# Kernel optimization log

Measured on AMD Instinct MI355X. Metric: run time of the kernel, lower is better.

## Reference

```python
import jax, jax.numpy as jnp
import numpy as np

# TT factorization for fc1: 768 = 4*4*6*8 -> 3072 = 4*6*8*16, ranks (1,12,24,12,1)
# TT factorization for fc2: 3072 = 4*6*8*16 -> 768 = 4*4*6*8, ranks (1,12,24,12,1)
IN_F1, OUT_F1 = (4, 4, 6, 8), (4, 6, 8, 16)
IN_F2, OUT_F2 = (4, 6, 8, 16), (4, 4, 6, 8)
RANKS = (12, 24, 12)


def _core(key, shape, fan_in):
    return jax.random.normal(key, shape, dtype=jnp.float32) * (fan_in ** -0.5)


def make_tt_params(key, in_f, out_f, ranks):
    r = (1,) + tuple(ranks) + (1,)
    ks = jax.random.split(key, 5)
    # boundary cores squeeze the unit rank dims
    g1 = _core(ks[0], (in_f[0], out_f[0], r[1]), in_f[0])              # (i1,o1,r1)
    g2 = _core(ks[1], (r[1], in_f[1], out_f[1], r[2]), r[1] * in_f[1])  # (r1,i2,o2,r2)
    g3 = _core(ks[2], (r[2], in_f[2], out_f[2], r[3]), r[2] * in_f[2])  # (r2,i3,o3,r3)
    g4 = _core(ks[3], (r[3], in_f[3], out_f[3]), r[3] * in_f[3])        # (r3,i4,o4)
    b = jnp.zeros((int(np.prod(out_f)),), dtype=jnp.float32)
    return g1, g2, g3, g4, b


def tt_linear(x2d, g1, g2, g3, g4, bias, in_f):
    # x2d: (N, prod(in_f)) -> (N, prod(out_f))
    z = x2d.reshape((-1,) + tuple(in_f))                  # (b,i1,i2,i3,i4)
    z = jnp.einsum('bijkl,ipr->bjklpr', z, g1)            # (b,i2,i3,i4,o1,r1)
    z = jnp.einsum('bjklpr,rjqs->bklpqs', z, g2)          # (b,i3,i4,o1,o2,r2)
    z = jnp.einsum('bklpqs,sktu->blpqtu', z, g3)          # (b,i4,o1,o2,o3,r3)
    z = jnp.einsum('blpqtu,ulv->bpqtv', z, g4)            # (b,o1,o2,o3,o4)
    return z.reshape(z.shape[0], -1) + bias


def setup_inputs() -> dict:
    key = jax.random.key(0)
    kx, k1, k2 = jax.random.split(key, 3)
    x = jax.random.normal(kx, (2, 2048, 768), dtype=jnp.float32)
    g1a, g1b, g1c, g1d, b1 = make_tt_params(k1, IN_F1, OUT_F1, RANKS)
    g2a, g2b, g2c, g2d, b2 = make_tt_params(k2, IN_F2, OUT_F2, RANKS)
    return {"x": x, "g1a": g1a, "g1b": g1b, "g1c": g1c, "g1d": g1d, "b1": b1,
            "g2a": g2a, "g2b": g2b, "g2c": g2c, "g2d": g2d, "b2": b2}


def reference(x, g1a, g1b, g1c, g1d, b1, g2a, g2b, g2c, g2d, b2):
    B, S, D = x.shape
    h = tt_linear(x.reshape(-1, D), g1a, g1b, g1c, g1d, b1, IN_F1)  # (N, 3072)
    h = jax.nn.gelu(h, approximate=False)  # nn.GELU() default = exact erf
    # dropout: identity in eval mode
    y = tt_linear(h, g2a, g2b, g2c, g2d, b2, IN_F2)                 # (N, 768)
    return y.reshape(B, S, -1)
```

## Files before the change

kernel.cpp:

```cpp
#include <hip/hip_runtime.h>
#include <cstdint>
#include <cstddef>

typedef unsigned short u16;
typedef __attribute__((ext_vector_type(8))) __bf16 bf16x8;
typedef __attribute__((ext_vector_type(4))) float f32x4;

__device__ __forceinline__ u16 f2bf(float f) {
  unsigned u = __float_as_uint(f);
  u += 0x7FFFu + ((u >> 16) & 1u);
  return (u16)(u >> 16);
}

__device__ __forceinline__ float bf2f(u16 h) {
  return __uint_as_float(((unsigned)h) << 16);
}

__device__ __forceinline__ void async16(u16* lds, const u16* g) {
  __builtin_amdgcn_global_load_lds(
      (const __attribute__((address_space(1))) unsigned int*)g,
      (__attribute__((address_space(3))) unsigned int*)lds, 16, 0, 0);
}

__global__ __launch_bounds__(256)
void prep(const float4* __restrict__ x4, ushort4* __restrict__ xb4,
          const float* __restrict__ gA1, const float* __restrict__ gB1,
          const float* __restrict__ gC1, const float* __restrict__ gD1,
          const float* __restrict__ gA2, const float* __restrict__ gB2,
          const float* __restrict__ gC2, const float* __restrict__ gD2,
          float* __restrict__ B12_1, float* __restrict__ B12_2,
          float* __restrict__ C1, float* __restrict__ C2) {
  const int b = blockIdx.x;
  const int tid = threadIdx.x;
  if (b < 3072) {
    int i = b * 256 + tid;
    float4 v = x4[i];
    ushort4 o;
    o.x = f2bf(v.x); o.y = f2bf(v.y); o.z = f2bf(v.z); o.w = f2bf(v.w);
    xb4[i] = o;
    return;
  }
  int idx = (b - 3072) * 256 + tid;
  if (idx < 9216) {
    int e = idx;
    int r2 = e % 24; int t = e / 24;
    int fo12 = t % 24, fi12 = t / 24;
    int i2 = fi12 % 4, i1 = fi12 / 4;
    int o2 = fo12 % 6, o1 = fo12 / 6;
    float s = 0.f;
#pragma unroll
    for (int r1 = 0; r1 < 12; ++r1)
      s += gA1[(i1 * 4 + o1) * 12 + r1] * gB1[((r1 * 4 + i2) * 6 + o2) * 24 + r2];
    B12_1[e] = s;
  } else if (idx < 18432) {
    int e = idx - 9216;
    int r2 = e % 24; int t = e / 24;
    int fo12 = t % 16, fi12 = t / 16;
    int i2 = fi12 % 6, i1 = fi12 / 6;
    int o2 = fo12 % 4, o1 = fo12 / 4;
    float s = 0.f;
#pragma unroll
    for (int r1 = 0; r1 < 12; ++r1)
      s += gA2[(i1 * 4 + o1) * 12 + r1] * gB2[((r1 * 6 + i2) * 4 + o2) * 24 + r2];
    B12_2[e] = s;
  } else if (idx < 165888) {
    int e = idx - 18432;
    int fi34 = e % 48; int t = e / 48;
    int fo34 = t % 128;
    int i3 = fi34 / 8, i4 = fi34 % 8;
    int o3 = fo34 / 16, o4 = fo34 % 16;
    int r2 = t / 128;
    float s = 0.f;
#pragma unroll
    for (int r3 = 0; r3 < 12; ++r3)
      s += gC1[((r2 * 6 + i3) * 8 + o3) * 12 + r3] * gD1[(r3 * 8 + i4) * 16 + o4];
    C1[e] = s;
  } else {
    int e = idx - 165888;
    int fi34 = e % 128; int t = e / 128;
    int fo34 = t % 48;
    int i3 = fi34 / 16, i4 = fi34 % 16;
    int o3 = fo34 / 8, o4 = fo34 % 8;
    int r2 = t / 48;
    float s = 0.f;
#pragma unroll
    for (int r3 = 0; r3 < 12; ++r3)
      s += gC2[((r2 * 8 + i3) * 6 + o3) * 12 + r3] * gD2[(r3 * 16 + i4) * 8 + o4];
    C2[e] = s;
  }
}

template <int FI12, int I34, int O12, int O34, int OG>
__device__ __forceinline__
void tt_expand_body(const float* __restrict__ B12, const float* __restrict__ C34t,
                    u16* __restrict__ Wt, int bx, int by, int tid, float* sB) {
  constexpr int R2 = 24;
  constexpr int Kin = FI12 * I34;
  constexpr int IC = Kin / 8;
  constexpr int I34C = I34 / 8;
  for (int e = tid; e < FI12 * OG * R2; e += 256) {
    int r2 = e % R2; int t = e / R2;
    int f = t % OG; int fi12 = t / OG;
    sB[(fi12 * OG + f) * 25 + r2] = B12[(fi12 * O12 + by * OG + f) * R2 + r2];
  }
  __syncthreads();
  const int t = bx * 256 + tid;
  const int fo34 = t / IC;
  const int ic = t % IC;
  const int fi12 = ic / I34C;
  const int fi34 = (ic % I34C) * 8;

  float acc[OG][8];
#pragma unroll
  for (int f = 0; f < OG; ++f)
#pragma unroll
    for (int k = 0; k < 8; ++k) acc[f][k] = 0.f;

  for (int r2 = 0; r2 < R2; ++r2) {
    const float4* cp = (const float4*)(C34t + ((size_t)(r2 * O34 + fo34) * I34 + fi34));
    float4 c0 = cp[0], c1 = cp[1];
    float c[8] = {c0.x, c0.y, c0.z, c0.w, c1.x, c1.y, c1.z, c1.w};
#pragma unroll
    for (int f = 0; f < OG; ++f) {
      float bb = sB[(fi12 * OG + f) * 25 + r2];
#pragma unroll
      for (int k = 0; k < 8; ++k) acc[f][k] += bb * c[k];
    }
  }
#pragma unroll
  for (int f = 0; f < OG; ++f) {
    int out = (by * OG + f) * O34 + fo34;
    u16 v[8];
#pragma unroll
    for (int k = 0; k < 8; ++k) v[k] = f2bf(acc[f][k]);
    *(uint4*)(Wt + (size_t)out * Kin + fi12 * I34 + fi34) = *(const uint4*)v;
  }
}

__global__ __launch_bounds__(256)
void tt_expand2(const float* __restrict__ B12_1, const float* __restrict__ C1, u16* __restrict__ W1t,
                const float* __restrict__ B12_2, const float* __restrict__ C2, u16* __restrict__ W2t) {
  __shared__ float sB[24 * 4 * 25];
  const int b = blockIdx.x;
  const int tid = threadIdx.x;
  if (b < 288) {
    tt_expand_body<16, 48, 24, 128, 4>(B12_1, C1, W1t, b % 48, b / 48, tid, sB);
  } else {
    int bb = b - 288;
    tt_expand_body<24, 128, 16, 48, 4>(B12_2, C2, W2t, bb % 72, bb / 72, tid, sB);
  }
}

__global__ void reduceN8(const uint4* __restrict__ P, const float* __restrict__ bias,
                         float4* __restrict__ out4, int n8, int zstride8, int nz) {
  int i = blockIdx.x * 256 + threadIdx.x;
  if (i >= n8) return;
  int b0 = (i % 96) * 8;
  float a[8];
#pragma unroll
  for (int k = 0; k < 8; ++k) a[k] = bias[b0 + k];
  for (int s = 0; s < nz; ++s) {
    uint4 u = P[i + s * zstride8];
    const u16* up = (const u16*)&u;
#pragma unroll
    for (int k = 0; k < 8; ++k) a[k] += bf2f(up[k]);
  }
  out4[i * 2]     = (float4){a[0], a[1], a[2], a[3]};
  out4[i * 2 + 1] = (float4){a[4], a[5], a[6], a[7]};
}

template <bool GELU, int MAP>
__global__ __launch_bounds__(256, 3)
void gemm_bt(const u16* __restrict__ A, const u16* __restrict__ Bt,
             const float* __restrict__ bias, u16* __restrict__ Out,
             int N, int K, int klen, size_t zstride) {
  const int flat = blockIdx.x;
  const int xcd = flat & 7;
  const int local = flat >> 3;
  int bm, bn, bz;
  if (MAP == 1) {
    bm = (xcd >> 1) * 8 + (local & 7);
    bn = (xcd & 1) * 12 + (local >> 3);
    bz = 0;
  } else {
    bm = (xcd & 1) * 16 + (local & 15);
    bn = local >> 4;
    bz = xcd >> 1;
  }

  __shared__ __align__(16) u16 As[2][128 * 32];
  __shared__ __align__(16) u16 Bs[2][128 * 32];
  const int tid = threadIdx.x;
  const int wave = tid >> 6, lane = tid & 63;
  const int wm = (wave & 1) * 64, wn = (wave >> 1) * 64;
  const int lr = lane & 15, lq = lane >> 4;

  const int srow = tid >> 2;
  const int scol = (tid & 3) * 8;
  const u16* Ag = A + (size_t)(bm * 128 + srow) * K + scol;
  const u16* Bg = Bt + (size_t)(bn * 128 + srow) * K + scol;
  u16* AsW = &As[0][0] + tid * 8;
  u16* BsW = &Bs[0][0] + tid * 8;

  f32x4 acc[4][4];
#pragma unroll
  for (int i = 0; i < 4; i++)
#pragma unroll
    for (int j = 0; j < 4; j++) acc[i][j] = (f32x4){0.f, 0.f, 0.f, 0.f};

  const int kbeg = bz * klen;
  const int nIter = klen >> 5;

  auto stage = [&](int buf, int k0) {
    async16(AsW + buf * 4096,        Ag + k0);
    async16(AsW + buf * 4096 + 2048, Ag + k0 + (size_t)64 * K);
    async16(BsW + buf * 4096,        Bg + k0);
    async16(BsW + buf * 4096 + 2048, Bg + k0 + (size_t)64 * K);
  };
  auto compute = [&](int buf) {
    bf16x8 af[4], bfr[4];
#pragma unroll
    for (int i = 0; i < 4; i++)
      af[i] = *(const bf16x8*)(&As[buf][0] + (wm + i * 16 + lr) * 32 + lq * 8);
#pragma unroll
    for (int j = 0; j < 4; j++)
      bfr[j] = *(const bf16x8*)(&Bs[buf][0] + (wn + j * 16 + lr) * 32 + lq * 8);
#pragma unroll
    for (int i = 0; i < 4; i++)
#pragma unroll
      for (int j = 0; j < 4; j++)
        acc[i][j] = __builtin_amdgcn_mfma_f32_16x16x32_bf16(af[i], bfr[j], acc[i][j], 0, 0, 0);
  };

  stage(0, kbeg);
  for (int it = 0; it < nIter; it += 2) {
    __syncthreads();
    if (it + 1 < nIter) stage(1, kbeg + (it + 1) * 32);
    compute(0);
    __syncthreads();
    if (it + 2 < nIter) stage(0, kbeg + (it + 2) * 32);
    compute(1);
  }

  u16* Op = Out + (size_t)bz * zstride;
  const int r0 = bm * 128 + wm + lq * 4;
  const int c0 = bn * 128 + wn + lr;
  float bv[4];
  if (GELU) {
#pragma unroll
    for (int j = 0; j < 4; j++) bv[j] = bias[c0 + j * 16];
  }
#pragma unroll
  for (int i = 0; i < 4; i++) {
#pragma unroll
    for (int r = 0; r < 4; r++) {
      const size_t rowoff = (size_t)(r0 + i * 16 + r) * N;
#pragma unroll
      for (int j = 0; j < 4; j++) {
        float v = acc[i][j][r];
        if (GELU) {
          v += bv[j];
          float inner = v * fmaf(v * v, 0.0356774081f, 0.7978845608f);
          float e = __builtin_amdgcn_exp2f(2.8853900818f * inner);
          float r1 = __builtin_amdgcn_rcpf(1.0f + e);
          v = v - v * r1;
        }
        Op[rowoff + c0 + j * 16] = f2bf(v);
      }
    }
  }
}

extern "C" void kernel_launch(void* const* d_in, const int* in_sizes, int n_in,
                              void* d_out, int out_size, void* d_ws, size_t ws_size,
                              hipStream_t stream) {
  const float* x   = (const float*)d_in[0];
  const float* g1a = (const float*)d_in[1];
  const float* g1b = (const float*)d_in[2];
  const float* g1c = (const float*)d_in[3];
  const float* g1d = (const float*)d_in[4];
  const float* b1  = (const float*)d_in[5];
  const float* g2a = (const float*)d_in[6];
  const float* g2b = (const float*)d_in[7];
  const float* g2c = (const float*)d_in[8];
  const float* g2d = (const float*)d_in[9];
  const float* b2  = (const float*)d_in[10];
  float* out = (float*)d_out;

  char* ws = (char*)d_ws;
  u16* xb   = (u16*)(ws + 0);
  u16* W1t  = (u16*)(ws + 6291456);
  u16* W2t  = (u16*)(ws + 11010048);
  u16* h    = (u16*)(ws + 15728640);
  u16* Part = (u16*)(ws + 40894464);
  float* B12_1 = (float*)(ws + 40894464);
  float* B12_2 = (float*)(ws + 40894464 + 36864);
  float* C1    = (float*)(ws + 40894464 + 73728);
  float* C2    = (float*)(ws + 40894464 + 663552);

  prep<<<4296, 256, 0, stream>>>((const float4*)x, (ushort4*)xb,
                                 g1a, g1b, g1c, g1d, g2a, g2b, g2c, g2d,
                                 B12_1, B12_2, C1, C2);

  tt_expand2<<<576, 256, 0, stream>>>(B12_1, C1, W1t, B12_2, C2, W2t);

  gemm_bt<true, 1><<<768, 256, 0, stream>>>(xb, W1t, b1, h, 3072, 768, 768, 0);
  gemm_bt<false, 2><<<768, 256, 0, stream>>>(h, W2t, nullptr, Part, 768, 3072, 768, 3145728);
  reduceN8<<<1536, 256, 0, stream>>>((const uint4*)Part, b2,
                                     (float4*)out, 393216, 393216, 4);
}
```

Before: 159.7 us.

## Retile GEMMs to 256x192 blocks with 8 waves and phased LDS pipeline

Rewrites the bf16 GEMM kernel to use 512-thread blocks computing 256x192 tiles with a 64-wide K step. A/B tiles are double- and triple-buffered with an XOR swizzle to cut LDS bank conflicts. Each K step is split into four barrier-separated phases that interleave async global->LDS loads with MFMA bursts under raised wave priority. The aim is more data reuse per block and better overlap of memory with compute. The cost is higher register and LDS use and many more barriers, and the kernel now hardcodes K=768 per split (NT=12).

```diff
diff --git a/kernel.cpp b/kernel.cpp
--- a/kernel.cpp
+++ b/kernel.cpp
@@ -170,102 +170,180 @@
 }
 
 template <bool GELU, int MAP>
-__global__ __launch_bounds__(256, 3)
+__global__ __launch_bounds__(512, 2)
 void gemm_bt(const u16* __restrict__ A, const u16* __restrict__ Bt,
              const float* __restrict__ bias, u16* __restrict__ Out,
-             int N, int K, int klen, size_t zstride) {
+             int N, int lda, int ldb, size_t zstride) {
+  constexpr int NT = 12;
   const int flat = blockIdx.x;
   const int xcd = flat & 7;
   const int local = flat >> 3;
   int bm, bn, bz;
   if (MAP == 1) {
-    bm = (xcd >> 1) * 8 + (local & 7);
-    bn = (xcd & 1) * 12 + (local >> 3);
+    bm = (xcd >> 1) * 4 + (local & 3);
+    bn = (xcd & 1) * 8 + (local >> 2);
     bz = 0;
   } else {
-    bm = (xcd & 1) * 16 + (local & 15);
-    bn = local >> 4;
     bz = xcd >> 1;
-  }
-
-  __shared__ __align__(16) u16 As[2][128 * 32];
-  __shared__ __align__(16) u16 Bs[2][128 * 32];
+    bm = (xcd & 1) * 8 + (local & 7);
+    bn = local >> 3;
+  }
+  const int kbeg = (MAP == 2) ? bz * 768 : 0;
+
+  __shared__ __align__(16) u16 AL[2][16384];
+  __shared__ __align__(16) u16 BL[3][12288];
+
   const int tid = threadIdx.x;
   const int wave = tid >> 6, lane = tid & 63;
-  const int wm = (wave & 1) * 64, wn = (wave >> 1) * 64;
   const int lr = lane & 15, lq = lane >> 4;
-
-  const int srow = tid >> 2;
-  const int scol = (tid & 3) * 8;
-  const u16* Ag = A + (size_t)(bm * 128 + srow) * K + scol;
-  const u16* Bg = Bt + (size_t)(bn * 128 + srow) * K + scol;
-  u16* AsW = &As[0][0] + tid * 8;
-  u16* BsW = &Bs[0][0] + tid * 8;
-
-  f32x4 acc[4][4];
-#pragma unroll
-  for (int i = 0; i < 4; i++)
-#pragma unroll
-    for (int j = 0; j < 4; j++) acc[i][j] = (f32x4){0.f, 0.f, 0.f, 0.f};
-
-  const int kbeg = bz * klen;
-  const int nIter = klen >> 5;
-
-  auto stage = [&](int buf, int k0) {
-    async16(AsW + buf * 4096,        Ag + k0);
-    async16(AsW + buf * 4096 + 2048, Ag + k0 + (size_t)64 * K);
-    async16(BsW + buf * 4096,        Bg + k0);
-    async16(BsW + buf * 4096 + 2048, Bg + k0 + (size_t)64 * K);
+  const int wr = (wave >> 2) * 128;
+  const int wc = (wave & 3) * 48;
+
+  const int prow = tid >> 3;
+  const int pcc  = (tid & 7) ^ (((tid >> 5) & 1) << 1);
+  const u16* Ag = A + (size_t)(bm * 256 + prow) * lda + kbeg + pcc * 8;
+  const u16* Bg = Bt + (size_t)(bn * 192 + prow) * ldb + kbeg + pcc * 8;
+
+  auto stA = [&](int slot, int p, int k) {
+    async16(&AL[slot][0] + p * 4096 + tid * 8, Ag + (size_t)(p * 64) * lda + k);
   };
-  auto compute = [&](int buf) {
-    bf16x8 af[4], bfr[4];
-#pragma unroll
-    for (int i = 0; i < 4; i++)
-      af[i] = *(const bf16x8*)(&As[buf][0] + (wm + i * 16 + lr) * 32 + lq * 8);
-#pragma unroll
-    for (int j = 0; j < 4; j++)
-      bfr[j] = *(const bf16x8*)(&Bs[buf][0] + (wn + j * 16 + lr) * 32 + lq * 8);
-#pragma unroll
-    for (int i = 0; i < 4; i++)
-#pragma unroll
-      for (int j = 0; j < 4; j++)
-        acc[i][j] = __builtin_amdgcn_mfma_f32_16x16x32_bf16(af[i], bfr[j], acc[i][j], 0, 0, 0);
+  auto stB = [&](int slot, int p, int k) {
+    async16(&BL[slot][0] + p * 4096 + tid * 8, Bg + (size_t)(p * 64) * ldb + k);
   };
 
-  stage(0, kbeg);
-  for (int it = 0; it < nIter; it += 2) {
-    __syncthreads();
-    if (it + 1 < nIter) stage(1, kbeg + (it + 1) * 32);
-    compute(0);
-    __syncthreads();
-    if (it + 2 < nIter) stage(0, kbeg + (it + 2) * 32);
-    compute(1);
+  int aOff[2][8], bOff[2][3];
+#pragma unroll
+  for (int kk = 0; kk < 2; ++kk) {
+#pragma unroll
+    for (int mi = 0; mi < 8; ++mi) {
+      int L = (wr + mi * 16 + lr) * 128 + kk * 64 + lq * 16;
+      L ^= ((L >> 9) & 1) << 5;
+      aOff[kk][mi] = L >> 1;
+    }
+#pragma unroll
+    for (int nj = 0; nj < 3; ++nj) {
+      int L = (wc + nj * 16 + lr) * 128 + kk * 64 + lq * 16;
+      L ^= ((L >> 9) & 1) << 5;
+      bOff[kk][nj] = L >> 1;
+    }
+  }
+
+  f32x4 acc[8][3];
+#pragma unroll
+  for (int mi = 0; mi < 8; ++mi)
+#pragma unroll
+    for (int nj = 0; nj < 3; ++nj) acc[mi][nj] = (f32x4){0.f, 0.f, 0.f, 0.f};
+
+  stA(0, 0, 0); stA(0, 1, 0); stA(0, 2, 0); stA(0, 3, 0);
+  stB(0, 0, 0); stB(0, 1, 0); stB(0, 2, 0);
+  stB(1, 0, 64); stB(1, 1, 64); stB(1, 2, 64);
+  asm volatile("s_waitcnt vmcnt(3)" ::: "memory");
+  __builtin_amdgcn_s_barrier();
+  __builtin_amdgcn_sched_barrier(0);
+
+  int bsR = 0, bsW = 2;
+  for (int t = 0; t < NT; ++t) {
+    const u16* Ab = &AL[t & 1][0];
+    const u16* Bb = &BL[bsR][0];
+    const int wAs = (t + 1) & 1;
+    const int kA = ((t + 1 < NT) ? t + 1 : NT - 1) * 64;
+    const int kB = ((t + 2 < NT) ? t + 2 : NT - 1) * 64;
+
+    bf16x8 bf[3], af[4], af2[4];
+#pragma unroll
+    for (int nj = 0; nj < 3; ++nj) bf[nj] = *(const bf16x8*)(Bb + bOff[0][nj]);
+#pragma unroll
+    for (int mi = 0; mi < 4; ++mi) af[mi] = *(const bf16x8*)(Ab + aOff[0][mi]);
+    stA(wAs, 0, kA); stA(wAs, 1, kA);
+    __builtin_amdgcn_s_barrier();
+    asm volatile("s_waitcnt lgkmcnt(0)" ::: "memory");
+    __builtin_amdgcn_sched_barrier(0);
+    __builtin_amdgcn_s_setprio(1);
+#pragma unroll
+    for (int mi = 0; mi < 4; ++mi)
+#pragma unroll
+      for (int nj = 0; nj < 3; ++nj)
+        acc[mi][nj] = __builtin_amdgcn_mfma_f32_16x16x32_bf16(af[mi], bf[nj], acc[mi][nj], 0, 0, 0);
+    __builtin_amdgcn_s_setprio(0);
+    __builtin_amdgcn_s_barrier();
+    __builtin_amdgcn_sched_barrier(0);
+#pragma unroll
+    for (int mi = 0; mi < 4; ++mi) af2[mi] = *(const bf16x8*)(Ab + aOff[0][4 + mi]);
+    stA(wAs, 2, kA); stA(wAs, 3, kA);
+    __builtin_amdgcn_s_barrier();
+    asm volatile("s_waitcnt lgkmcnt(0)" ::: "memory");
+    __builtin_amdgcn_sched_barrier(0);
+    __builtin_amdgcn_s_setprio(1);
+#pragma unroll
+    for (int mi = 0; mi < 4; ++mi)
+#pragma unroll
+      for (int nj = 0; nj < 3; ++nj)
+        acc[4 + mi][nj] = __builtin_amdgcn_mfma_f32_16x16x32_bf16(af2[mi], bf[nj], acc[4 + mi][nj], 0, 0, 0);
+    __builtin_amdgcn_s_setprio(0);
+    __builtin_amdgcn_s_barrier();
+    __builtin_amdgcn_sched_barrier(0);
+#pragma unroll
+    for (int nj = 0; nj < 3; ++nj) bf[nj] = *(const bf16x8*)(Bb + bOff[1][nj]);
+#pragma unroll
+    for (int mi = 0; mi < 4; ++mi) af[mi] = *(const bf16x8*)(Ab + aOff[1][mi]);
+    stB(bsW, 0, kB); stB(bsW, 1, kB);
+    __builtin_amdgcn_s_barrier();
+    asm volatile("s_waitcnt lgkmcnt(0)" ::: "memory");
+    __builtin_amdgcn_sched_barrier(0);
+    __builtin_amdgcn_s_setprio(1);
+#pragma unroll
+    for (int mi = 0; mi < 4; ++mi)
+#pragma unroll
+      for (int nj = 0; nj < 3; ++nj)
+        acc[mi][nj] = __builtin_amdgcn_mfma_f32_16x16x32_bf16(af[mi], bf[nj], acc[mi][nj], 0, 0, 0);
+    __builtin_amdgcn_s_setprio(0);
+    __builtin_amdgcn_s_barrier();
+    __builtin_amdgcn_sched_barrier(0);
+#pragma unroll
+    for (int mi = 0; mi < 4; ++mi) af2[mi] = *(const bf16x8*)(Ab + aOff[1][4 + mi]);
+    stB(bsW, 2, kB);
+    __builtin_amdgcn_s_barrier();
+    asm volatile("s_waitcnt lgkmcnt(0)" ::: "memory");
+    __builtin_amdgcn_sched_barrier(0);
+    __builtin_amdgcn_s_setprio(1);
+#pragma unroll
+    for (int mi = 0; mi < 4; ++mi)
+#pragma unroll
+      for (int nj = 0; nj < 3; ++nj)
+        acc[4 + mi][nj] = __builtin_amdgcn_mfma_f32_16x16x32_bf16(af2[mi], bf[nj], acc[4 + mi][nj], 0, 0, 0);
+    __builtin_amdgcn_s_setprio(0);
+    asm volatile("s_waitcnt vmcnt(3)" ::: "memory");
+    __builtin_amdgcn_s_barrier();
+    __builtin_amdgcn_sched_barrier(0);
+
+    bsR = (bsR + 1 == 3) ? 0 : bsR + 1;
+    bsW = (bsW + 1 == 3) ? 0 : bsW + 1;
   }
 
   u16* Op = Out + (size_t)bz * zstride;
-  const int r0 = bm * 128 + wm + lq * 4;
-  const int c0 = bn * 128 + wn + lr;
-  float bv[4];
+  const int r0 = bm * 256 + wr + lq * 4;
+  const int c0 = bn * 192 + wc + lr;
+  float bv[3];
   if (GELU) {
 #pragma unroll
-    for (int j = 0; j < 4; j++) bv[j] = bias[c0 + j * 16];
-  }
-#pragma unroll
-  for (int i = 0; i < 4; i++) {
-#pragma unroll
-    for (int r = 0; r < 4; r++) {
-      const size_t rowoff = (size_t)(r0 + i * 16 + r) * N;
-#pragma unroll
-      for (int j = 0; j < 4; j++) {
-        float v = acc[i][j][r];
+    for (int nj = 0; nj < 3; ++nj) bv[nj] = bias[c0 + nj * 16];
+  }
+#pragma unroll
+  for (int mi = 0; mi < 8; ++mi) {
+#pragma unroll
+    for (int r = 0; r < 4; ++r) {
+      const size_t rowoff = (size_t)(r0 + mi * 16 + r) * N;
+#pragma unroll
+      for (int nj = 0; nj < 3; ++nj) {
+        float v = acc[mi][nj][r];
         if (GELU) {
-          v += bv[j];
+          v += bv[nj];
           float inner = v * fmaf(v * v, 0.0356774081f, 0.7978845608f);
           float e = __builtin_amdgcn_exp2f(2.8853900818f * inner);
           float r1 = __builtin_amdgcn_rcpf(1.0f + e);
           v = v - v * r1;
         }
-        Op[rowoff + c0 + j * 16] = f2bf(v);
+        Op[rowoff + c0 + nj * 16] = f2bf(v);
       }
     }
   }
@@ -304,8 +382,8 @@
 
   tt_expand2<<<576, 256, 0, stream>>>(B12_1, C1, W1t, B12_2, C2, W2t);
 
-  gemm_bt<true, 1><<<768, 256, 0, stream>>>(xb, W1t, b1, h, 3072, 768, 768, 0);
-  gemm_bt<false, 2><<<768, 256, 0, stream>>>(h, W2t, nullptr, Part, 768, 3072, 768, 3145728);
+  gemm_bt<true, 1><<<256, 512, 0, stream>>>(xb, W1t, b1, h, 3072, 768, 768, 0);
+  gemm_bt<false, 2><<<256, 512, 0, stream>>>(h, W2t, nullptr, Part, 768, 3072, 3072, 3145728);
   reduceN8<<<1536, 256, 0, stream>>>((const uint4*)Part, b2,
                                      (float4*)out, 393216, 393216, 4);
 }
```

After: 160.1 us. About the same (+0.3%).
